# Kernel optimization log

Measured on AMD Instinct MI355X. Metric: run time of the kernel, lower is better.

## Reference

```python
import jax, jax.numpy as jnp
import numpy as np

EMB, HEADS, DEPTH, SEQ, BATCH = 256, 8, 4, 8192, 4
DH = EMB // HEADS  # 32
FF = 4 * EMB
EPS = 1e-5


def setup_inputs() -> dict:
    key = jax.random.key(0)
    ks = jax.random.split(key, 8)
    w = lambda k, shape: jax.random.normal(k, shape, dtype=jnp.float32) * 0.02
    D = DEPTH
    return {
        "x": jax.random.normal(ks[0], (BATCH, SEQ, EMB), dtype=jnp.float32),
        "Wq": w(ks[1], (D, EMB, EMB)),
        "Wk": w(ks[2], (D, EMB, EMB)),
        "Wv": w(ks[3], (D, EMB, EMB)),
        "Wo": w(ks[4], (D, EMB, EMB)),
        "bo": jnp.zeros((D, EMB), jnp.float32),
        "ln1_g": jnp.ones((D, EMB), jnp.float32),
        "ln1_b": jnp.zeros((D, EMB), jnp.float32),
        "W1": w(ks[5], (D, EMB, FF)),
        "b1": jnp.zeros((D, FF), jnp.float32),
        "W2": w(ks[6], (D, FF, EMB)),
        "b2": jnp.zeros((D, EMB), jnp.float32),
        "ln2_g": jnp.ones((D, EMB), jnp.float32),
        "ln2_b": jnp.zeros((D, EMB), jnp.float32),
    }


def _layernorm(x, g, b):
    mu = x.mean(-1, keepdims=True)
    var = ((x - mu) ** 2).mean(-1, keepdims=True)
    return (x - mu) * jax.lax.rsqrt(var + EPS) * g + b


def _linear_attn(x, Wq, Wk, Wv, Wo, bo):
    # lucidrains linear_attn: q,k scaled by d**-0.25; softmax q over feature dim,
    # k over sequence dim; context = k^T v (per head), out = q @ context.
    b, n, dm = x.shape
    split = lambda t: t.reshape(b, n, HEADS, DH).transpose(0, 2, 1, 3)  # -> bhnd
    scale = DH ** -0.25
    q = jax.nn.softmax(split(x @ Wq) * scale, axis=-1)   # over d
    k = jax.nn.softmax(split(x @ Wk) * scale, axis=-2)   # over n
    v = split(x @ Wv)
    context = jnp.einsum('bhnd,bhne->bhde', k, v)        # [b,h,d,d]
    out = jnp.einsum('bhnd,bhde->bhne', q, context)      # [b,h,n,d]
    out = out.transpose(0, 2, 1, 3).reshape(b, n, dm)
    return out @ Wo + bo


def _forward(x, Wq, Wk, Wv, Wo, bo, ln1_g, ln1_b, W1, b1, W2, b2, ln2_g, ln2_b):
    for i in range(DEPTH):
        h = _layernorm(x, ln1_g[i], ln1_b[i])
        x = x + _linear_attn(h, Wq[i], Wk[i], Wv[i], Wo[i], bo[i])
        h = _layernorm(x, ln2_g[i], ln2_b[i])
        x = x + (jax.nn.gelu(h @ W1[i] + b1[i], approximate=False) @ W2[i] + b2[i])
    return x


def reference(x, Wq, Wk, Wv, Wo, bo, ln1_g, ln1_b, W1, b1, W2, b2, ln2_g, ln2_b):
    return _forward(x, Wq, Wk, Wv, Wo, bo, ln1_g, ln1_b, W1, b1, W2, b2, ln2_g, ln2_b)
```

## Files before the change

kernel.cpp:

```cpp
#include <hip/hip_runtime.h>
#include <hip/hip_bf16.h>

typedef __attribute__((ext_vector_type(8))) short bf16x8;
typedef __attribute__((ext_vector_type(4))) float f32x4;

#define EMB 256
#define HEADS 8
#define DH 32
#define SEQ 8192
#define BATCH 4
#define NROWS (SEQ*BATCH)
#define FFD 1024
#define DEPTH 4
#define QKVN 768
#define SCALE 0.42044820762685725f
#define NCHUNK 128
#define ROWS_PER_CHUNK (SEQ/NCHUNK)

static __device__ __forceinline__ float bf2f(ushort u){
  union { unsigned int i; float f; } x; x.i = ((unsigned int)u) << 16; return x.f;
}
static __device__ __forceinline__ ushort f2bf(float f){
  union { __hip_bfloat16 h; ushort u; } cv;
  cv.h = __float2bfloat16(f);
  return cv.u;
}
static __device__ __forceinline__ float gelu_f(float v){
  float y = 0.7978845608028654f * (v + 0.044715f*v*v*v);
  float e = __expf(2.0f*y);
  return 0.5f*v*(1.0f + (1.0f - 2.0f/(e + 1.0f)));
}

static __device__ __forceinline__ void gload_lds16(const ushort* g, ushort* l){
  __builtin_amdgcn_global_load_lds(
      (const __attribute__((address_space(1))) unsigned int*)(uintptr_t)g,
      (__attribute__((address_space(3))) unsigned int*)(uintptr_t)l,
      16, 0, 0);
}

__global__ __launch_bounds__(256) void prep_weights(
    const float* __restrict__ Wq, const float* __restrict__ Wk,
    const float* __restrict__ Wv, const float* __restrict__ Wo,
    const float* __restrict__ W1, const float* __restrict__ W2,
    ushort* __restrict__ wqkv_t, ushort* __restrict__ wo_t,
    ushort* __restrict__ w1_t, ushort* __restrict__ w2_t)
{
  __shared__ float tile[32][33];
  int bid = blockIdx.x;
  int L = bid / 768, r = bid % 768;
  const float* src; ushort* dst; int K, N, tidx;
  if (r < 192){ int which = r >> 6; tidx = r & 63;
    src = (which==0?Wq:which==1?Wk:Wv) + (long)L*65536;
    dst = wqkv_t + (long)L*QKVN*EMB + which*EMB*EMB; K=256; N=256;
  } else if (r < 256){ tidx = r-192; src = Wo + (long)L*65536; dst = wo_t + (long)L*65536; K=256; N=256; }
  else if (r < 512){ tidx = r-256; src = W1 + (long)L*262144; dst = w1_t + (long)L*262144; K=256; N=1024; }
  else { tidx = r-512; src = W2 + (long)L*262144; dst = w2_t + (long)L*262144; K=1024; N=256; }
  int tn = N >> 5;
  int tk = tidx / tn, tj = tidx % tn;
  int k0 = tk*32, n0 = tj*32;
  int c = threadIdx.x & 31, r0 = threadIdx.x >> 5;
  #pragma unroll
  for (int i=0;i<4;i++){
    int rr = r0 + i*8;
    tile[rr][c] = src[(long)(k0+rr)*N + n0 + c];
  }
  __syncthreads();
  #pragma unroll
  for (int i=0;i<4;i++){
    int rr = r0 + i*8;
    dst[(long)(n0+rr)*K + k0 + c] = f2bf(tile[c][rr]);
  }
}

__global__ void copy_f4(const float4* __restrict__ src, float4* __restrict__ dst, int n4){
  int i = blockIdx.x*blockDim.x + threadIdx.x;
  int stride = gridDim.x*blockDim.x;
  for (; i < n4; i += stride) dst[i] = src[i];
}

__global__ __launch_bounds__(256) void ln_kernel(const float* __restrict__ x,
    const float* __restrict__ g, const float* __restrict__ bb,
    ushort* __restrict__ h)
{
  int wid = threadIdx.x >> 6, lane = threadIdx.x & 63;
  long row = (long)blockIdx.x*4 + wid;
  const float4 xv = *(const float4*)(x + row*EMB + lane*4);
  float s = xv.x+xv.y+xv.z+xv.w;
  float s2 = xv.x*xv.x+xv.y*xv.y+xv.z*xv.z+xv.w*xv.w;
  #pragma unroll
  for (int m=1;m<64;m<<=1){ s += __shfl_xor(s,m,64); s2 += __shfl_xor(s2,m,64); }
  float mean = s * (1.0f/EMB);
  float inv = rsqrtf(s2*(1.0f/EMB) - mean*mean + 1e-5f);
  float4 gv = *(const float4*)(g + lane*4);
  float4 bv = *(const float4*)(bb + lane*4);
  ushort4 o;
  o.x = f2bf((xv.x-mean)*inv*gv.x + bv.x);
  o.y = f2bf((xv.y-mean)*inv*gv.y + bv.y);
  o.z = f2bf((xv.z-mean)*inv*gv.z + bv.z);
  o.w = f2bf((xv.w-mean)*inv*gv.w + bv.w);
  *(ushort4*)(h + row*EMB + lane*4) = o;
}

template<int MODE, int BN>
__global__ __launch_bounds__(512, 2) void gemm_bt(
    const ushort* __restrict__ A, const ushort* __restrict__ Bt,
    int M, int N, int K,
    const float* __restrict__ bias,
    float* __restrict__ xres, ushort* __restrict__ outb)
{
  constexpr int BM = 256, BK = 64;
  constexpr int NF = BN/64;
  __shared__ ushort LDSraw[2*BM*BK + 2*BN*BK];
  ushort* Abuf0 = LDSraw;
  ushort* Abuf1 = LDSraw + BM*BK;
  ushort* Bbuf0 = LDSraw + 2*BM*BK;
  ushort* Bbuf1 = LDSraw + 2*BM*BK + BN*BK;
  int t = threadIdx.x;
  int lane = t & 63, wid = t >> 6;
  int wr = wid >> 2, wc = wid & 3;
  int wrb = wr*128, wcb = wc*(BN/4);
  long rowA0 = (long)blockIdx.x * BM;
  long colB0 = (long)blockIdx.y * BN;
  const ushort* gA[4]; int dA[4];
  #pragma unroll
  for (int i=0;i<4;i++){
    int row = i*64 + (t>>3);
    int clog = (t&7) ^ (row&7);
    gA[i] = A + (rowA0 + row)*(long)K + clog*8;
    dA[i] = (i*512 + t)*8;
  }
  const ushort* gB[NF]; int dB[NF];
  #pragma unroll
  for (int i=0;i<NF;i++){
    int row = i*64 + (t>>3);
    int clog = (t&7) ^ (row&7);
    gB[i] = Bt + (colB0 + row)*(long)K + clog*8;
    dB[i] = (i*512 + t)*8;
  }
  ushort* Ac = Abuf0; ushort* An = Abuf1;
  ushort* Bc = Bbuf0; ushort* Bn = Bbuf1;
  f32x4 acc[8][NF] = {};
  int fr = lane & 15, cr4 = lane >> 4, xr = fr & 7;
  int nsteps = K >> 6;
  #pragma unroll
  for (int i=0;i<4;i++) gload_lds16(gA[i], Ac + dA[i]);
  #pragma unroll
  for (int i=0;i<NF;i++) gload_lds16(gB[i], Bc + dB[i]);
  asm volatile("s_waitcnt vmcnt(0)" ::: "memory");
  __syncthreads();
  for (int s = 0; s < nsteps; ++s){
    bool pf = (s+1 < nsteps);
    long knext = (long)(s+1) << 6;
    #pragma unroll
    for (int kk=0; kk<2; ++kk){
      int chunk = ((kk*4 + cr4) ^ xr) << 3;
      bf16x8 bv[NF];
      #pragma unroll
      for (int n=0;n<NF;n++)
        bv[n] = *(const bf16x8*)(Bc + (wcb + n*16 + fr)*BK + chunk);
      #pragma unroll
      for (int mh=0; mh<2; ++mh){
        bf16x8 av[4];
        #pragma unroll
        for (int m=0;m<4;m++)
          av[m] = *(const bf16x8*)(Ac + (wrb + (mh*4+m)*16 + fr)*BK + chunk);
        if (pf){
          if (kk==0 && mh==0){ gload_lds16(gA[0]+knext, An+dA[0]); gload_lds16(gA[1]+knext, An+dA[1]); }
          if (kk==0 && mh==1){ gload_lds16(gA[2]+knext, An+dA[2]); gload_lds16(gA[3]+knext, An+dA[3]); }
          if (kk==1 && mh==0){ gload_lds16(gB[0]+knext, Bn+dB[0]); if (NF>2) gload_lds16(gB[1]+knext, Bn+dB[1]); }
          if (kk==1 && mh==1){
            if (NF>2){ gload_lds16(gB[2]+knext, Bn+dB[2]); gload_lds16(gB[3]+knext, Bn+dB[3]); }
            else     { gload_lds16(gB[1]+knext, Bn+dB[1]); }
          }
        }
        __builtin_amdgcn_s_setprio(1);
        #pragma unroll
        for (int m=0;m<4;m++){
          #pragma unroll
          for (int n=0;n<NF;n++)
            acc[mh*4+m][n] = __builtin_amdgcn_mfma_f32_16x16x32_bf16(av[m], bv[n], acc[mh*4+m][n], 0,0,0);
        }
        __builtin_amdgcn_s_setprio(0);
      }
    }
    asm volatile("s_waitcnt vmcnt(0)" ::: "memory");
    __syncthreads();
    ushort* tp;
    tp = Ac; Ac = An; An = tp;
    tp = Bc; Bc = Bn; Bn = tp;
  }
  constexpr int BNP = BN + 4;
  float* bounce = (float*)LDSraw;
  int fq = lane >> 4;
  int rdrow = t / (BN/4);
  int rdcol = (t % (BN/4)) * 4;
  constexpr int RPP = 512 / (BN/4);
  #pragma unroll
  for (int r = 0; r < 4; ++r){
    __syncthreads();
    if (wr == (r>>1)){
      int mb = (r&1)*4;
      #pragma unroll
      for (int m4=0;m4<4;m4++){
        #pragma unroll
        for (int n=0;n<NF;n++){
          #pragma unroll
          for (int i=0;i<4;i++)
            bounce[(m4*16 + fq*4 + i)*BNP + wcb + n*16 + fr] = acc[mb+m4][n][i];
        }
      }
    }
    __syncthreads();
    long gr0 = rowA0 + r*64;
    #pragma unroll
    for (int p=0;p<64/RPP;p++){
      int lr = p*RPP + rdrow;
      long gr = gr0 + lr;
      long gc = colB0 + rdcol;
      float4 v = *(float4*)&bounce[lr*BNP + rdcol];
      if (MODE==0){
        ushort4 o; o.x=f2bf(v.x); o.y=f2bf(v.y); o.z=f2bf(v.z); o.w=f2bf(v.w);
        *(ushort4*)&outb[gr*N + gc] = o;
      } else if (MODE==1){
        const float4 bv4 = *(const float4*)&bias[gc];
        float4 xv = *(float4*)&xres[gr*N + gc];
        xv.x += v.x + bv4.x; xv.y += v.y + bv4.y;
        xv.z += v.z + bv4.z; xv.w += v.w + bv4.w;
        *(float4*)&xres[gr*N + gc] = xv;
      } else {
        const float4 bv4 = *(const float4*)&bias[gc];
        ushort4 o;
        o.x = f2bf(gelu_f(v.x + bv4.x)); o.y = f2bf(gelu_f(v.y + bv4.y));
        o.z = f2bf(gelu_f(v.z + bv4.z)); o.w = f2bf(gelu_f(v.w + bv4.w));
        *(ushort4*)&outb[gr*N + gc] = o;
      }
    }
  }
}

__global__ __launch_bounds__(256) void colstats_partial(const ushort* __restrict__ qkv,
    float* __restrict__ pmax, float* __restrict__ psum)
{
  int ch = blockIdx.x, b = blockIdx.y;
  int t = threadIdx.x;
  const ushort* base = qkv + ((long)b*SEQ + (long)ch*ROWS_PER_CHUNK)*QKVN + EMB + t;
  float m[4] = {-1e30f,-1e30f,-1e30f,-1e30f};
  float s[4] = {0.f,0.f,0.f,0.f};
  #pragma unroll 2
  for (int n = 0; n < ROWS_PER_CHUNK; n += 4){
    #pragma unroll
    for (int j=0;j<4;j++){
      float v = bf2f(base[(long)(n+j)*QKVN]) * SCALE;
      float m2 = fmaxf(m[j], v);
      s[j] = s[j]*__expf(m[j]-m2) + __expf(v-m2);
      m[j] = m2;
    }
  }
  float M = fmaxf(fmaxf(m[0],m[1]), fmaxf(m[2],m[3]));
  float S = s[0]*__expf(m[0]-M) + s[1]*__expf(m[1]-M)
          + s[2]*__expf(m[2]-M) + s[3]*__expf(m[3]-M);
  long idx = ((long)b*NCHUNK + ch)*EMB + t;
  pmax[idx] = M; psum[idx] = S;
}

__global__ __launch_bounds__(256) void colstats_reduce(const float* __restrict__ pmax,
    const float* __restrict__ psum, float* __restrict__ kmax, float* __restrict__ ksum)
{
  int b = blockIdx.x, t = threadIdx.x;
  const float* pm = pmax + (long)b*NCHUNK*EMB + t;
  const float* ps = psum + (long)b*NCHUNK*EMB + t;
  float m = -1e30f, s = 0.f;
  for (int c = 0; c < NCHUNK; ++c){
    float cm = pm[(long)c*EMB], cs = ps[(long)c*EMB];
    float m2 = fmaxf(m, cm);
    s = s*__expf(m-m2) + cs*__expf(cm-m2);
    m = m2;
  }
  kmax[b*EMB + t] = m;
  ksum[b*EMB + t] = s;
}

__global__ __launch_bounds__(256) void ctx_partial(
    const ushort* __restrict__ qkv, const float* __restrict__ kmax,
    float* __restrict__ ctx_part)
{
  constexpr int LT = 72;
  __shared__ ushort ekT[32*LT];
  __shared__ ushort vvT[32*LT];
  int ch = blockIdx.x, h = blockIdx.y, b = blockIdx.z;
  int t = threadIdx.x, lane = t & 63, wid = t >> 6;
  long nbase = (long)b*SEQ + ch*512;
  int lrow = t >> 2, lseg = (t & 3) << 3;
  float km[8];
  #pragma unroll
  for (int j=0;j<8;j++) km[j] = kmax[b*256 + h*DH + lseg + j];
  int wstep = wid & 1, wdr = (wid >> 1) << 4;
  f32x4 acc0 = {}, acc1 = {};
  int frow = lane & 15, g8 = (lane >> 4) << 3;
  for (int st = 0; st < 8; ++st){
    long n0 = nbase + st*64;
    const ushort* gk = qkv + (n0 + lrow)*QKVN + EMB + h*DH + lseg;
    uint4 kv = *(const uint4*)gk;
    uint4 vv = *(const uint4*)(gk + EMB);
    __syncthreads();
    const ushort* kp = (const ushort*)&kv;
    const ushort* vp = (const ushort*)&vv;
    #pragma unroll
    for (int j=0;j<8;j++){
      float f = bf2f(kp[j])*SCALE;
      ekT[(lseg+j)*LT + lrow] = f2bf(__expf(f - km[j]));
      vvT[(lseg+j)*LT + lrow] = vp[j];
    }
    __syncthreads();
    bf16x8 afr = *(const bf16x8*)(ekT + (wdr + frow)*LT + wstep*32 + g8);
    bf16x8 bf0 = *(const bf16x8*)(vvT + frow*LT + wstep*32 + g8);
    bf16x8 bf1 = *(const bf16x8*)(vvT + (16 + frow)*LT + wstep*32 + g8);
    acc0 = __builtin_amdgcn_mfma_f32_16x16x32_bf16(afr, bf0, acc0, 0,0,0);
    acc1 = __builtin_amdgcn_mfma_f32_16x16x32_bf16(afr, bf1, acc1, 0,0,0);
  }
  int fq = lane >> 4;
  long pb = (((long)(b*HEADS+h))*32 + (ch*2+wstep))*1024;
  #pragma unroll
  for (int i=0;i<4;i++){
    ctx_part[pb + (wdr + fq*4 + i)*32 + frow] = acc0[i];
    ctx_part[pb + (wdr + fq*4 + i)*32 + 16 + frow] = acc1[i];
  }
}

__global__ __launch_bounds__(256) void ctx_reduce(const float* __restrict__ ctx_part,
    const float* __restrict__ ksum, ushort* __restrict__ ctxT)
{
  int bh = blockIdx.x; int b = bh >> 3, h = bh & 7;
  int t = threadIdx.x; int d = t >> 3, e4 = (t & 7) << 2;
  const float* p = ctx_part + (long)bh*32768 + d*32 + e4;
  float sx=0, sy=0, sz=0, sw=0;
  for (int c=0;c<32;c++){
    const float4 v = *(const float4*)(p + c*1024);
    sx+=v.x; sy+=v.y; sz+=v.z; sw+=v.w;
  }
  float inv = 1.0f / ksum[b*256 + h*DH + d];
  long base = (long)bh*1024;
  ctxT[base + (e4+0)*32 + d] = f2bf(sx*inv);
  ctxT[base + (e4+1)*32 + d] = f2bf(sy*inv);
  ctxT[base + (e4+2)*32 + d] = f2bf(sz*inv);
  ctxT[base + (e4+3)*32 + d] = f2bf(sw*inv);
}

__global__ __launch_bounds__(256) void attn_out(
    const ushort* __restrict__ qkv, const ushort* __restrict__ ctxT,
    ushort* __restrict__ ao)
{
  __shared__ ushort sq[4][16][264];
  int t = threadIdx.x, lane = t & 63, wid = t >> 6;
  long row0 = (long)blockIdx.x*64 + wid*16;
  int b = (int)(row0 / SEQ);
  int fr = lane & 15, g = lane >> 4;
  bf16x8 cf[8][2];
  #pragma unroll
  for (int h=0;h<8;h++){
    #pragma unroll
    for (int eh=0;eh<2;eh++)
      cf[h][eh] = *(const bf16x8*)(ctxT + ((long)(b*8+h)*32 + eh*16 + fr)*32 + g*8);
  }
  long gr = row0 + fr;
  #pragma unroll
  for (int hh=0;hh<2;hh++){
    int h = g*2 + hh;
    const ushort* qp = qkv + gr*QKVN + h*DH;
    union { uint4 v[4]; ushort u[32]; } qq;
    qq.v[0]=*(const uint4*)qp; qq.v[1]=*(const uint4*)(qp+8);
    qq.v[2]=*(const uint4*)(qp+16); qq.v[3]=*(const uint4*)(qp+24);
    float f[32]; float m = -1e30f;
    #pragma unroll
    for (int j=0;j<32;j++){ f[j] = bf2f(qq.u[j])*SCALE; m = fmaxf(m, f[j]); }
    float ssum = 0.f;
    #pragma unroll
    for (int j=0;j<32;j++){ f[j] = __expf(f[j]-m); ssum += f[j]; }
    float inv = 1.0f/ssum;
    union { uint4 v[4]; ushort u[32]; } oo;
    #pragma unroll
    for (int j=0;j<32;j++) oo.u[j] = f2bf(f[j]*inv);
    ushort* dst = &sq[wid][fr][h*DH];
    #pragma unroll
    for (int c2=0;c2<4;c2++) *(uint4*)(dst + c2*8) = oo.v[c2];
  }
  __syncthreads();
  #pragma unroll
  for (int h=0;h<8;h++){
    bf16x8 af = *(const bf16x8*)(&sq[wid][fr][h*DH + g*8]);
    f32x4 z = {};
    f32x4 o0 = __builtin_amdgcn_mfma_f32_16x16x32_bf16(af, cf[h][0], z, 0,0,0);
    f32x4 o1 = __builtin_amdgcn_mfma_f32_16x16x32_bf16(af, cf[h][1], z, 0,0,0);
    #pragma unroll
    for (int i=0;i<4;i++){
      long r = row0 + g*4 + i;
      ao[r*EMB + h*DH + fr]      = f2bf(o0[i]);
      ao[r*EMB + h*DH + 16 + fr] = f2bf(o1[i]);
    }
  }
}

extern "C" void kernel_launch(void* const* d_in, const int* in_sizes, int n_in,
                              void* d_out, int out_size, void* d_ws, size_t ws_size,
                              hipStream_t stream)
{
  const float* x_in = (const float*)d_in[0];
  const float* Wq  = (const float*)d_in[1];
  const float* Wk  = (const float*)d_in[2];
  const float* Wv  = (const float*)d_in[3];
  const float* Wo  = (const float*)d_in[4];
  const float* bo  = (const float*)d_in[5];
  const float* ln1g = (const float*)d_in[6];
  const float* ln1b = (const float*)d_in[7];
  const float* W1  = (const float*)d_in[8];
  const float* b1  = (const float*)d_in[9];
  const float* W2  = (const float*)d_in[10];
  const float* b2  = (const float*)d_in[11];
  const float* ln2g = (const float*)d_in[12];
  const float* ln2b = (const float*)d_in[13];
  float* x = (float*)d_out;

  char* ws = (char*)d_ws;
  ushort* h_buf  = (ushort*)ws;  ws += (long)NROWS*EMB*2;
  ushort* big    = (ushort*)ws;  ws += (long)NROWS*FFD*2;
  ushort* wqkv_t = (ushort*)ws;  ws += (long)DEPTH*QKVN*EMB*2;
  ushort* wo_t   = (ushort*)ws;  ws += (long)DEPTH*EMB*EMB*2;
  ushort* w1_t   = (ushort*)ws;  ws += (long)DEPTH*FFD*EMB*2;
  ushort* w2_t   = (ushort*)ws;  ws += (long)DEPTH*EMB*FFD*2;
  float*  kmax   = (float*)ws;   ws += (long)BATCH*EMB*4;
  float*  ksumv  = (float*)ws;   ws += (long)BATCH*EMB*4;
  float*  ctx_part = (float*)ws; ws += (long)BATCH*HEADS*32*1024*4;
  ushort* ctxT   = (ushort*)ws;  ws += (long)BATCH*HEADS*1024*2;
  float*  pmax   = (float*)ws;   ws += (long)BATCH*NCHUNK*EMB*4;
  float*  psum   = (float*)ws;   ws += (long)BATCH*NCHUNK*EMB*4;

  prep_weights<<<3072, 256, 0, stream>>>(Wq, Wk, Wv, Wo, W1, W2, wqkv_t, wo_t, w1_t, w2_t);
  copy_f4<<<2048, 256, 0, stream>>>((const float4*)x_in, (float4*)x, NROWS*EMB/4);

  ushort* qkv = big;
  ushort* ffb = big;
  for (int L = 0; L < DEPTH; ++L){
    ln_kernel<<<NROWS/4, 256, 0, stream>>>(x, ln1g + L*EMB, ln1b + L*EMB, h_buf);
    gemm_bt<0,128><<<dim3(NROWS/256, QKVN/128), 512, 0, stream>>>(
        h_buf, wqkv_t + (long)L*QKVN*EMB, NROWS, QKVN, EMB, nullptr, nullptr, qkv);
    colstats_partial<<<dim3(NCHUNK, BATCH), 256, 0, stream>>>(qkv, pmax, psum);
    colstats_reduce<<<BATCH, 256, 0, stream>>>(pmax, psum, kmax, ksumv);
    ctx_partial<<<dim3(16, HEADS, BATCH), 256, 0, stream>>>(qkv, kmax, ctx_part);
    ctx_reduce<<<32, 256, 0, stream>>>(ctx_part, ksumv, ctxT);
    attn_out<<<NROWS/64, 256, 0, stream>>>(qkv, ctxT, h_buf);
    gemm_bt<1,128><<<dim3(NROWS/256, EMB/128), 512, 0, stream>>>(
        h_buf, wo_t + (long)L*EMB*EMB, NROWS, EMB, EMB, bo + L*EMB, x, nullptr);
    ln_kernel<<<NROWS/4, 256, 0, stream>>>(x, ln2g + L*EMB, ln2b + L*EMB, h_buf);
    gemm_bt<2,256><<<dim3(NROWS/256, FFD/256), 512, 0, stream>>>(
        h_buf, w1_t + (long)L*FFD*EMB, NROWS, FFD, EMB, b1 + L*FFD, nullptr, ffb);
    gemm_bt<1,128><<<dim3(NROWS/256, EMB/128), 512, 0, stream>>>(
        ffb, w2_t + (long)L*EMB*FFD, NROWS, EMB, FFD, b2 + L*EMB, x, nullptr);
  }
}
```

Before: 704.5 us.

## Fuse residual add and LayerNorm into output-projection GEMM epilogues

Adds a GEMM epilogue mode that does the residual add and bias, writes x, then applies the next LayerNorm and writes the bf16 normalized activations. To do this each block covers full 256-wide rows, using a templated BM=128, BN=256 tile with a single column block. This removes the standalone LayerNorm launches inside the loop and the initial copy kernel: the first layer reads x_in as its residual source, and one LN runs up front. The cost is a heavier epilogue with wave-wide shuffles, a smaller M tile for the Wo and W2 GEMMs, and h_buf being read and overwritten by the same kernel.

```diff
diff --git a/kernel.cpp b/kernel.cpp
--- a/kernel.cpp
+++ b/kernel.cpp
@@ -72,12 +72,6 @@
   }
 }
 
-__global__ void copy_f4(const float4* __restrict__ src, float4* __restrict__ dst, int n4){
-  int i = blockIdx.x*blockDim.x + threadIdx.x;
-  int stride = gridDim.x*blockDim.x;
-  for (; i < n4; i += stride) dst[i] = src[i];
-}
-
 __global__ __launch_bounds__(256) void ln_kernel(const float* __restrict__ x,
     const float* __restrict__ g, const float* __restrict__ bb,
     ushort* __restrict__ h)
@@ -101,15 +95,22 @@
   *(ushort4*)(h + row*EMB + lane*4) = o;
 }
 
-template<int MODE, int BN>
+template<int MODE, int BM, int BN>
 __global__ __launch_bounds__(512, 2) void gemm_bt(
     const ushort* __restrict__ A, const ushort* __restrict__ Bt,
     int M, int N, int K,
     const float* __restrict__ bias,
-    float* __restrict__ xres, ushort* __restrict__ outb)
-{
-  constexpr int BM = 256, BK = 64;
+    const float* __restrict__ xin, float* __restrict__ xout,
+    ushort* __restrict__ outb,
+    const float* __restrict__ lng, const float* __restrict__ lnb)
+{
+  constexpr int BK = 64;
   constexpr int NF = BN/64;
+  constexpr int MR = BM/32;
+  constexpr int MH = MR/4;
+  constexpr int AI = BM/64;
+  constexpr int TI = AI + NF;
+  constexpr int NPH = 2*MH;
   __shared__ ushort LDSraw[2*BM*BK + 2*BN*BK];
   ushort* Abuf0 = LDSraw;
   ushort* Abuf1 = LDSraw + BM*BK;
@@ -118,12 +119,12 @@
   int t = threadIdx.x;
   int lane = t & 63, wid = t >> 6;
   int wr = wid >> 2, wc = wid & 3;
-  int wrb = wr*128, wcb = wc*(BN/4);
+  int wrb = wr*(BM/2), wcb = wc*(BN/4);
   long rowA0 = (long)blockIdx.x * BM;
   long colB0 = (long)blockIdx.y * BN;
-  const ushort* gA[4]; int dA[4];
-  #pragma unroll
-  for (int i=0;i<4;i++){
+  const ushort* gA[AI]; int dA[AI];
+  #pragma unroll
+  for (int i=0;i<AI;i++){
     int row = i*64 + (t>>3);
     int clog = (t&7) ^ (row&7);
     gA[i] = A + (rowA0 + row)*(long)K + clog*8;
@@ -139,11 +140,11 @@
   }
   ushort* Ac = Abuf0; ushort* An = Abuf1;
   ushort* Bc = Bbuf0; ushort* Bn = Bbuf1;
-  f32x4 acc[8][NF] = {};
+  f32x4 acc[MR][NF] = {};
   int fr = lane & 15, cr4 = lane >> 4, xr = fr & 7;
   int nsteps = K >> 6;
   #pragma unroll
-  for (int i=0;i<4;i++) gload_lds16(gA[i], Ac + dA[i]);
+  for (int i=0;i<AI;i++) gload_lds16(gA[i], Ac + dA[i]);
   #pragma unroll
   for (int i=0;i<NF;i++) gload_lds16(gB[i], Bc + dB[i]);
   asm volatile("s_waitcnt vmcnt(0)" ::: "memory");
@@ -159,18 +160,19 @@
       for (int n=0;n<NF;n++)
         bv[n] = *(const bf16x8*)(Bc + (wcb + n*16 + fr)*BK + chunk);
       #pragma unroll
-      for (int mh=0; mh<2; ++mh){
+      for (int mh=0; mh<MH; ++mh){
+        int sp = kk*MH + mh;
         bf16x8 av[4];
         #pragma unroll
         for (int m=0;m<4;m++)
           av[m] = *(const bf16x8*)(Ac + (wrb + (mh*4+m)*16 + fr)*BK + chunk);
         if (pf){
-          if (kk==0 && mh==0){ gload_lds16(gA[0]+knext, An+dA[0]); gload_lds16(gA[1]+knext, An+dA[1]); }
-          if (kk==0 && mh==1){ gload_lds16(gA[2]+knext, An+dA[2]); gload_lds16(gA[3]+knext, An+dA[3]); }
-          if (kk==1 && mh==0){ gload_lds16(gB[0]+knext, Bn+dB[0]); if (NF>2) gload_lds16(gB[1]+knext, Bn+dB[1]); }
-          if (kk==1 && mh==1){
-            if (NF>2){ gload_lds16(gB[2]+knext, Bn+dB[2]); gload_lds16(gB[3]+knext, Bn+dB[3]); }
-            else     { gload_lds16(gB[1]+knext, Bn+dB[1]); }
+          #pragma unroll
+          for (int j=0;j<TI;j++){
+            if (j*NPH >= sp*TI && j*NPH < (sp+1)*TI){
+              if (j < AI) gload_lds16(gA[j]+knext, An+dA[j]);
+              else        gload_lds16(gB[j-AI]+knext, Bn+dB[j-AI]);
+            }
           }
         }
         __builtin_amdgcn_s_setprio(1);
@@ -195,11 +197,12 @@
   int rdrow = t / (BN/4);
   int rdcol = (t % (BN/4)) * 4;
   constexpr int RPP = 512 / (BN/4);
-  #pragma unroll
-  for (int r = 0; r < 4; ++r){
+  constexpr int ROUNDS = BM/64;
+  #pragma unroll
+  for (int r = 0; r < ROUNDS; ++r){
     __syncthreads();
-    if (wr == (r>>1)){
-      int mb = (r&1)*4;
+    if (wr == r/(ROUNDS/2 > 0 ? ROUNDS/2 : 1)){
+      int mb = (ROUNDS==4) ? (r&1)*4 : 0;
       #pragma unroll
       for (int m4=0;m4<4;m4++){
         #pragma unroll
@@ -221,18 +224,32 @@
       if (MODE==0){
         ushort4 o; o.x=f2bf(v.x); o.y=f2bf(v.y); o.z=f2bf(v.z); o.w=f2bf(v.w);
         *(ushort4*)&outb[gr*N + gc] = o;
-      } else if (MODE==1){
-        const float4 bv4 = *(const float4*)&bias[gc];
-        float4 xv = *(float4*)&xres[gr*N + gc];
-        xv.x += v.x + bv4.x; xv.y += v.y + bv4.y;
-        xv.z += v.z + bv4.z; xv.w += v.w + bv4.w;
-        *(float4*)&xres[gr*N + gc] = xv;
-      } else {
+      } else if (MODE==2){
         const float4 bv4 = *(const float4*)&bias[gc];
         ushort4 o;
         o.x = f2bf(gelu_f(v.x + bv4.x)); o.y = f2bf(gelu_f(v.y + bv4.y));
         o.z = f2bf(gelu_f(v.z + bv4.z)); o.w = f2bf(gelu_f(v.w + bv4.w));
         *(ushort4*)&outb[gr*N + gc] = o;
+      } else {
+        const float4 bv4 = *(const float4*)&bias[gc];
+        const float4 xo  = *(const float4*)&xin[gr*N + gc];
+        v.x += bv4.x + xo.x; v.y += bv4.y + xo.y;
+        v.z += bv4.z + xo.z; v.w += bv4.w + xo.w;
+        *(float4*)&xout[gr*N + gc] = v;
+        float s1 = v.x+v.y+v.z+v.w;
+        float s2 = v.x*v.x+v.y*v.y+v.z*v.z+v.w*v.w;
+        #pragma unroll
+        for (int mm=1;mm<64;mm<<=1){ s1 += __shfl_xor(s1,mm,64); s2 += __shfl_xor(s2,mm,64); }
+        float mean = s1 * (1.0f/EMB);
+        float inv = rsqrtf(s2*(1.0f/EMB) - mean*mean + 1e-5f);
+        const float4 g4 = *(const float4*)&lng[gc];
+        const float4 b4 = *(const float4*)&lnb[gc];
+        ushort4 o;
+        o.x = f2bf((v.x-mean)*inv*g4.x + b4.x);
+        o.y = f2bf((v.y-mean)*inv*g4.y + b4.y);
+        o.z = f2bf((v.z-mean)*inv*g4.z + b4.z);
+        o.w = f2bf((v.w-mean)*inv*g4.w + b4.w);
+        *(ushort4*)&outb[gr*EMB + gc] = o;
       }
     }
   }
@@ -435,25 +452,30 @@
   float*  psum   = (float*)ws;   ws += (long)BATCH*NCHUNK*EMB*4;
 
   prep_weights<<<3072, 256, 0, stream>>>(Wq, Wk, Wv, Wo, W1, W2, wqkv_t, wo_t, w1_t, w2_t);
-  copy_f4<<<2048, 256, 0, stream>>>((const float4*)x_in, (float4*)x, NROWS*EMB/4);
+  ln_kernel<<<NROWS/4, 256, 0, stream>>>(x_in, ln1g, ln1b, h_buf);
 
   ushort* qkv = big;
   ushort* ffb = big;
   for (int L = 0; L < DEPTH; ++L){
-    ln_kernel<<<NROWS/4, 256, 0, stream>>>(x, ln1g + L*EMB, ln1b + L*EMB, h_buf);
-    gemm_bt<0,128><<<dim3(NROWS/256, QKVN/128), 512, 0, stream>>>(
-        h_buf, wqkv_t + (long)L*QKVN*EMB, NROWS, QKVN, EMB, nullptr, nullptr, qkv);
+    gemm_bt<0,256,128><<<dim3(NROWS/256, QKVN/128), 512, 0, stream>>>(
+        h_buf, wqkv_t + (long)L*QKVN*EMB, NROWS, QKVN, EMB,
+        nullptr, nullptr, nullptr, qkv, nullptr, nullptr);
     colstats_partial<<<dim3(NCHUNK, BATCH), 256, 0, stream>>>(qkv, pmax, psum);
     colstats_reduce<<<BATCH, 256, 0, stream>>>(pmax, psum, kmax, ksumv);
     ctx_partial<<<dim3(16, HEADS, BATCH), 256, 0, stream>>>(qkv, kmax, ctx_part);
     ctx_reduce<<<32, 256, 0, stream>>>(ctx_part, ksumv, ctxT);
     attn_out<<<NROWS/64, 256, 0, stream>>>(qkv, ctxT, h_buf);
-    gemm_bt<1,128><<<dim3(NROWS/256, EMB/128), 512, 0, stream>>>(
-        h_buf, wo_t + (long)L*EMB*EMB, NROWS, EMB, EMB, bo + L*EMB, x, nullptr);
-    ln_kernel<<<NROWS/4, 256, 0, stream>>>(x, ln2g + L*EMB, ln2b + L*EMB, h_buf);
-    gemm_bt<2,256><<<dim3(NROWS/256, FFD/256), 512, 0, stream>>>(
-        h_buf, w1_t + (long)L*FFD*EMB, NROWS, FFD, EMB, b1 + L*FFD, nullptr, ffb);
-    gemm_bt<1,128><<<dim3(NROWS/256, EMB/128), 512, 0, stream>>>(
-        ffb, w2_t + (long)L*EMB*FFD, NROWS, EMB, FFD, b2 + L*EMB, x, nullptr);
-  }
-}
+    gemm_bt<3,128,256><<<dim3(NROWS/128, 1), 512, 0, stream>>>(
+        h_buf, wo_t + (long)L*EMB*EMB, NROWS, EMB, EMB,
+        bo + L*EMB, (L==0 ? x_in : x), x, h_buf,
+        ln2g + L*EMB, ln2b + L*EMB);
+    gemm_bt<2,256,256><<<dim3(NROWS/256, FFD/256), 512, 0, stream>>>(
+        h_buf, w1_t + (long)L*FFD*EMB, NROWS, FFD, EMB,
+        b1 + L*FFD, nullptr, nullptr, ffb, nullptr, nullptr);
+    int Ln = (L+1 < DEPTH) ? (L+1) : 0;
+    gemm_bt<3,128,256><<<dim3(NROWS/128, 1), 512, 0, stream>>>(
+        ffb, w2_t + (long)L*EMB*FFD, NROWS, EMB, FFD,
+        b2 + L*EMB, x, x, h_buf,
+        ln1g + Ln*EMB, ln1b + Ln*EMB);
+  }
+}
```

Result: faster. 656.6 us (-6.8%).
